# Kernel tuning notes

Hardware: AMD Instinct MI355X
Metric: run time of the kernel (lower is better)

The kernel has to match this reference:

```python
import jax, jax.numpy as jnp
import numpy as np

WIN = 9  # window size per spatial dim (default [9,9,9] for 3D)


def _window_sum(x):
    # Depthwise conv with an all-ones [9,9,9] kernel, stride 1, zero pad 4
    # == sliding-window box sum. lax.reduce_window is the efficient, exact form.
    pad = WIN // 2
    return jax.lax.reduce_window(
        x, 0.0, jax.lax.add,
        window_dimensions=(1, 1, WIN, WIN, WIN),
        window_strides=(1, 1, 1, 1, 1),
        padding=((0, 0), (0, 0), (pad, pad), (pad, pad), (pad, pad)),
    )


def setup_inputs() -> dict:
    key = jax.random.key(0)
    k1, k2 = jax.random.split(key)
    shape = (2, 1, 160, 160, 160)  # [B, C, D, H, W]
    y_true = jax.random.normal(k1, shape, dtype=jnp.float32)
    y_pred = jax.random.normal(k2, shape, dtype=jnp.float32)
    return {"y_true": y_true, "y_pred": y_pred}


def reference(y_true, y_pred):
    Ii, Ji = y_true, y_pred
    win_size = jnp.asarray(WIN ** 3, dtype=Ii.dtype)  # 729

    I2 = Ii * Ii
    J2 = Ji * Ji
    IJ = Ii * Ji

    I_sum = _window_sum(Ii)
    J_sum = _window_sum(Ji)
    I2_sum = _window_sum(I2)
    J2_sum = _window_sum(J2)
    IJ_sum = _window_sum(IJ)

    u_I = I_sum / win_size
    u_J = J_sum / win_size

    cross = IJ_sum - u_J * I_sum - u_I * J_sum + u_I * u_J * win_size
    I_var = I2_sum - 2.0 * u_I * I_sum + u_I * u_I * win_size
    J_var = J2_sum - 2.0 * u_J * J_sum + u_J * u_J * win_size

    cc = cross * cross / (I_var * J_var + 1e-05)
    # mean over spatial dims [2,3,4] -> [B,C], then mean -> scalar
    return (1.0 - jnp.mean(cc, axis=(2, 3, 4))).mean()
```

## Files before the change

kernel.cpp:

```cpp
#include <hip/hip_runtime.h>


typedef float floatx2 __attribute__((ext_vector_type(2)));

constexpr int W = 160, H = 160, D = 160;
constexpr int SLICE = W * H;
constexpr int NVOX  = W * H * D;
constexpr int BATCH = 2;
constexpr int FROW  = 5 * W;
constexpr float RW  = 1.0f / 729.0f;

constexpr int TPB_P = 400;
constexpr int XT    = 80;
constexpr int NXT   = W / XT;
constexpr int CZ    = 80;
constexpr int NCZ   = D / CZ;
constexpr int ZS    = CZ + 8;
constexpr int NUNITS = ZS * 10;
constexpr int NBLK_P = BATCH * H * NXT * NCZ;

constexpr int TPB_Y = 448;
constexpr int YQ    = 40;
constexpr int NYQ   = H / YQ;
constexpr int YR    = YQ + 8;
constexpr int NBLK_Y = BATCH * D * NYQ;
constexpr int LDW   = YR * FROW / 16;

__device__ inline unsigned int pk4(float a, float b, float c, float d) {
    unsigned int u = 0;
    u = __builtin_amdgcn_cvt_pk_fp8_f32(a, b, u, false);
    u = __builtin_amdgcn_cvt_pk_fp8_f32(c, d, u, true);
    return u;
}
__device__ inline void up4(unsigned int v, float* o) {
    floatx2 t;
    t = __builtin_amdgcn_cvt_pk_f32_fp8(v, false); o[0] = t[0]; o[1] = t[1];
    t = __builtin_amdgcn_cvt_pk_f32_fp8(v, true);  o[2] = t[0]; o[3] = t[1];
}
__device__ inline void up8(uint2 v, float* o) {
    up4(v.x, o); up4(v.y, o + 4);
}

__global__ __launch_bounds__(TPB_P) void pass_pzx(const float* __restrict__ I,
                                                  const float* __restrict__ J,
                                                  unsigned char* __restrict__ outA) {
    __shared__ unsigned char xw[5][ZS][XT];

    int blk = blockIdx.x;
    int zc = blk % NCZ;
    int xt = (blk / NCZ) % NXT;
    int y  = (blk / (NCZ * NXT)) % H;
    int b  = blk / (NCZ * NXT * H);
    int tx0 = xt * XT;
    int zbase = zc * CZ - 4;
    const float* Ib = I + (size_t)b * NVOX + y * W;
    const float* Jb = J + (size_t)b * NVOX + y * W;

    const float4 Z4 = make_float4(0.f, 0.f, 0.f, 0.f);
    for (int u = threadIdx.x; u < NUNITS; u += TPB_P) {
        int zs = u / 10;
        int xu = u % 10;
        int gxs = tx0 + xu * 8;
        int gz = zbase + zs;
        float a[16], c[16];
        if (gz >= 0 && gz < D) {
            const float* ip = Ib + (size_t)gz * SLICE + gxs;
            const float* jp = Jb + (size_t)gz * SLICE + gxs;
            float4 A0 = (gxs >= 4)     ? *(const float4*)(ip - 4) : Z4;
            float4 A1 = *(const float4*)(ip);
            float4 A2 = *(const float4*)(ip + 4);
            float4 A3 = (gxs + 11 < W) ? *(const float4*)(ip + 8) : Z4;
            float4 C0 = (gxs >= 4)     ? *(const float4*)(jp - 4) : Z4;
            float4 C1 = *(const float4*)(jp);
            float4 C2 = *(const float4*)(jp + 4);
            float4 C3 = (gxs + 11 < W) ? *(const float4*)(jp + 8) : Z4;
            float at[16] = {A0.x,A0.y,A0.z,A0.w, A1.x,A1.y,A1.z,A1.w,
                            A2.x,A2.y,A2.z,A2.w, A3.x,A3.y,A3.z,A3.w};
            float ct[16] = {C0.x,C0.y,C0.z,C0.w, C1.x,C1.y,C1.z,C1.w,
                            C2.x,C2.y,C2.z,C2.w, C3.x,C3.y,C3.z,C3.w};
#pragma unroll
            for (int k = 0; k < 16; ++k) { a[k] = at[k]; c[k] = ct[k]; }
        } else {
#pragma unroll
            for (int k = 0; k < 16; ++k) { a[k] = 0.f; c[k] = 0.f; }
        }
#pragma unroll
        for (int f = 0; f < 5; ++f) {
            float v[16];
#pragma unroll
            for (int k = 0; k < 16; ++k) {
                float x = a[k], yv = c[k];
                v[k] = (f == 0) ? x : (f == 1) ? yv :
                       (f == 2) ? x * x : (f == 3) ? yv * yv : x * yv;
            }
            float P[16];
            P[0] = v[0];
#pragma unroll
            for (int k = 1; k < 16; ++k) P[k] = P[k - 1] + v[k];
            float w[8];
            w[0] = P[8];
#pragma unroll
            for (int j = 1; j < 8; ++j) w[j] = P[j + 8] - P[j - 1];
            uint2 pk;
            pk.x = pk4(w[0], w[1], w[2], w[3]);
            pk.y = pk4(w[4], w[5], w[6], w[7]);
            *(uint2*)&xw[f][zs][xu * 8] = pk;
        }
    }

    __syncthreads();

    {
        int xg = threadIdx.x % 20;
        int zl = threadIdx.x / 20;
        int x0l = xg * 4;
        int zo0 = zl * 4;

        float acc[5][4];
#pragma unroll
        for (int f = 0; f < 5; ++f)
#pragma unroll
            for (int i = 0; i < 4; ++i) acc[f][i] = 0.f;

#pragma unroll
        for (int k = 0; k < 9; ++k) {
#pragma unroll
            for (int f = 0; f < 5; ++f) {
                unsigned int v = *(const unsigned int*)&xw[f][zo0 + k][x0l];
                float u[4]; up4(v, u);
                acc[f][0] += u[0]; acc[f][1] += u[1];
                acc[f][2] += u[2]; acc[f][3] += u[3];
            }
        }

        int gz0 = zc * CZ + zo0;
        unsigned char* op = outA + ((size_t)(b * D + gz0) * H + y) * FROW + tx0 + x0l;
#pragma unroll
        for (int q = 0; q < 4; ++q) {
#pragma unroll
            for (int f = 0; f < 5; ++f)
                *(unsigned int*)(op + f * W) =
                    pk4(acc[f][0], acc[f][1], acc[f][2], acc[f][3]);
            if (q < 3) {
#pragma unroll
                for (int f = 0; f < 5; ++f) {
                    unsigned int ve = *(const unsigned int*)&xw[f][zo0 + 9 + q][x0l];
                    unsigned int vl = *(const unsigned int*)&xw[f][zo0 + q][x0l];
                    float ue[4], ul[4];
                    up4(ve, ue); up4(vl, ul);
                    acc[f][0] += ue[0] - ul[0]; acc[f][1] += ue[1] - ul[1];
                    acc[f][2] += ue[2] - ul[2]; acc[f][3] += ue[3] - ul[3];
                }
                op += (size_t)H * FROW;
            }
        }
    }
}

__global__ __launch_bounds__(TPB_Y) void pass_y2(const unsigned char* __restrict__ A,
                                                 double* __restrict__ partials) {
    __shared__ unsigned char rows[YR * FROW];
    __shared__ double sm[TPB_Y / 64];

    int blk = blockIdx.x;
    int yq = blk % NYQ;
    int z  = (blk / NYQ) % D;
    int b  = blk / (NYQ * D);
    int y0 = yq * YQ;
    int tid = threadIdx.x;
    const unsigned char* __restrict__ src =
        A + ((size_t)(b * D + z) * H) * FROW;

    for (int i = tid; i < LDW; i += TPB_Y) {
        int off = i * 16;
        int r = off / FROW;
        int gy = y0 - 4 + r;
        uint4 v = make_uint4(0u, 0u, 0u, 0u);
        if (gy >= 0 && gy < H)
            v = *(const uint4*)(src + (size_t)gy * FROW + (off % FROW));
        *(uint4*)&rows[off] = v;
    }
    __syncthreads();

    double acc = 0.0;
    if (tid < 400) {
        int xg = tid % 20;
        int ys = tid / 20;
        int rbase = ys * 2;
        int x8 = xg * 8;

        float s[5][8];
#pragma unroll
        for (int f = 0; f < 5; ++f)
#pragma unroll
            for (int i = 0; i < 8; ++i) s[f][i] = 0.f;

#pragma unroll
        for (int t = 0; t < 9; ++t) {
            const unsigned char* rp = &rows[(rbase + t) * FROW + x8];
#pragma unroll
            for (int f = 0; f < 5; ++f) {
                uint2 v = *(const uint2*)(rp + f * W);
                float u[8]; up8(v, u);
#pragma unroll
                for (int i = 0; i < 8; ++i) s[f][i] += u[i];
            }
        }

#pragma unroll
        for (int o = 0; o < 2; ++o) {
            float rowcc = 0.f;
#pragma unroll
            for (int i = 0; i < 8; ++i) {
                float Is = s[0][i], Js = s[1][i];
                float I2s = s[2][i], J2s = s[3][i], IJs = s[4][i];
                float tI = RW * Is;
                float cross = __builtin_fmaf(-tI, Js, IJs);
                float Iv    = __builtin_fmaf(-tI, Is, I2s);
                float Jv    = __builtin_fmaf(-(RW * Js), Js, J2s);
                float den   = __builtin_fmaf(Iv, Jv, 1e-5f);
                rowcc = __builtin_fmaf(cross * cross, __builtin_amdgcn_rcpf(den), rowcc);
            }
            acc += (double)rowcc;
            if (o == 0) {
                const unsigned char* re = &rows[(rbase + 9) * FROW + x8];
                const unsigned char* rl = &rows[rbase * FROW + x8];
#pragma unroll
                for (int f = 0; f < 5; ++f) {
                    uint2 ve = *(const uint2*)(re + f * W);
                    uint2 vl = *(const uint2*)(rl + f * W);
                    float ue[8], ul[8];
                    up8(ve, ue); up8(vl, ul);
#pragma unroll
                    for (int i = 0; i < 8; ++i) s[f][i] += ue[i] - ul[i];
                }
            }
        }
    }

#pragma unroll
    for (int off = 32; off > 0; off >>= 1) acc += __shfl_down(acc, off);
    if ((tid & 63) == 0) sm[tid >> 6] = acc;
    __syncthreads();
    if (tid == 0) {
        double tt = 0.0;
#pragma unroll
        for (int i = 0; i < TPB_Y / 64; ++i) tt += sm[i];
        partials[blockIdx.x] = tt;
    }
}

__global__ __launch_bounds__(256) void finalize(const double* __restrict__ p,
                                                float* __restrict__ out) {
    double v = 0.0;
    for (int i = threadIdx.x; i < NBLK_Y; i += 256) v += p[i];
#pragma unroll
    for (int off = 32; off > 0; off >>= 1) v += __shfl_down(v, off);
    __shared__ double sm[4];
    int lane = threadIdx.x & 63, wid = threadIdx.x >> 6;
    if (lane == 0) sm[wid] = v;
    __syncthreads();
    if (threadIdx.x == 0) {
        double tt = 0.0;
#pragma unroll
        for (int i = 0; i < 4; ++i) tt += sm[i];
        out[0] = (float)(1.0 - tt / (double)((double)BATCH * (double)NVOX));
    }
}

extern "C" void kernel_launch(void* const* d_in, const int* in_sizes, int n_in,
                              void* d_out, int out_size, void* d_ws, size_t ws_size,
                              hipStream_t stream) {
    const float* I = (const float*)d_in[0];
    const float* J = (const float*)d_in[1];
    float* out = (float*)d_out;

    size_t bufsz = ((size_t)BATCH * 5 * NVOX + 255) / 256 * 256;
    unsigned char* bufA = (unsigned char*)d_ws;
    double* partials = (double*)(bufA + bufsz);

    pass_pzx<<<NBLK_P, TPB_P, 0, stream>>>(I, J, bufA);
    pass_y2<<<NBLK_Y, TPB_Y, 0, stream>>>(bufA, partials);
    finalize<<<1, 256, 0, stream>>>(partials, out);
}
```

Before: 59.64 us.

## Reorder separable box-sum passes: fuse x,y in first pass, do z in second

The first pass now computes the x and y window sums within a single z-slice, reading contiguous rows of a slice instead of strided columns across z. The second pass then does the z window sum and the loss reduction, loading 48 z-planes of one y-row from the fp8 intermediate. This turns the large strided float reads in the first pass into contiguous slice reads. In exchange, the second pass now gathers its rows with a large stride across z from the intermediate buffer.

```diff
diff --git a/kernel.cpp b/kernel.cpp
--- a/kernel.cpp
+++ b/kernel.cpp
@@ -11,20 +11,17 @@
 constexpr float RW  = 1.0f / 729.0f;
 
 constexpr int TPB_P = 400;
-constexpr int XT    = 80;
-constexpr int NXT   = W / XT;
-constexpr int CZ    = 80;
-constexpr int NCZ   = D / CZ;
-constexpr int ZS    = CZ + 8;
-constexpr int NUNITS = ZS * 10;
-constexpr int NBLK_P = BATCH * H * NXT * NCZ;
-
-constexpr int TPB_Y = 448;
-constexpr int YQ    = 40;
-constexpr int NYQ   = H / YQ;
-constexpr int YR    = YQ + 8;
-constexpr int NBLK_Y = BATCH * D * NYQ;
-constexpr int LDW   = YR * FROW / 16;
+constexpr int CHY   = 40, NCHY = H / CHY;
+constexpr int YS    = CHY + 8;
+constexpr int NUNITS = YS * 20;
+constexpr int NBLK_P = BATCH * D * NCHY;
+
+constexpr int TPB_Z2 = 448;
+constexpr int ZQ    = 40;
+constexpr int NZQ   = D / ZQ;
+constexpr int ZR    = ZQ + 8;
+constexpr int NBLK_Z2 = BATCH * H * NZQ;
+constexpr int LDW   = ZR * FROW / 16;
 
 __device__ inline unsigned int pk4(float a, float b, float c, float d) {
     unsigned int u = 0;
@@ -41,31 +38,29 @@
     up4(v.x, o); up4(v.y, o + 4);
 }
 
-__global__ __launch_bounds__(TPB_P) void pass_pzx(const float* __restrict__ I,
+__global__ __launch_bounds__(TPB_P) void pass_pxy(const float* __restrict__ I,
                                                   const float* __restrict__ J,
                                                   unsigned char* __restrict__ outA) {
-    __shared__ unsigned char xw[5][ZS][XT];
+    __shared__ unsigned char xw[5][YS][W];
 
     int blk = blockIdx.x;
-    int zc = blk % NCZ;
-    int xt = (blk / NCZ) % NXT;
-    int y  = (blk / (NCZ * NXT)) % H;
-    int b  = blk / (NCZ * NXT * H);
-    int tx0 = xt * XT;
-    int zbase = zc * CZ - 4;
-    const float* Ib = I + (size_t)b * NVOX + y * W;
-    const float* Jb = J + (size_t)b * NVOX + y * W;
+    int yc = blk % NCHY;
+    int z  = (blk / NCHY) % D;
+    int b  = blk / (NCHY * D);
+    int y0 = yc * CHY;
+    const float* Ib = I + (size_t)b * NVOX + (size_t)z * SLICE;
+    const float* Jb = J + (size_t)b * NVOX + (size_t)z * SLICE;
 
     const float4 Z4 = make_float4(0.f, 0.f, 0.f, 0.f);
     for (int u = threadIdx.x; u < NUNITS; u += TPB_P) {
-        int zs = u / 10;
-        int xu = u % 10;
-        int gxs = tx0 + xu * 8;
-        int gz = zbase + zs;
+        int r  = u / 20;
+        int xu = u % 20;
+        int gxs = xu * 8;
+        int gy = y0 - 4 + r;
         float a[16], c[16];
-        if (gz >= 0 && gz < D) {
-            const float* ip = Ib + (size_t)gz * SLICE + gxs;
-            const float* jp = Jb + (size_t)gz * SLICE + gxs;
+        if (gy >= 0 && gy < H) {
+            const float* ip = Ib + (size_t)gy * W + gxs;
+            const float* jp = Jb + (size_t)gy * W + gxs;
             float4 A0 = (gxs >= 4)     ? *(const float4*)(ip - 4) : Z4;
             float4 A1 = *(const float4*)(ip);
             float4 A2 = *(const float4*)(ip + 4);
@@ -104,17 +99,17 @@
             uint2 pk;
             pk.x = pk4(w[0], w[1], w[2], w[3]);
             pk.y = pk4(w[4], w[5], w[6], w[7]);
-            *(uint2*)&xw[f][zs][xu * 8] = pk;
+            *(uint2*)&xw[f][r][xu * 8] = pk;
         }
     }
 
     __syncthreads();
 
     {
-        int xg = threadIdx.x % 20;
-        int zl = threadIdx.x / 20;
+        int xg = threadIdx.x % 40;
+        int yl = threadIdx.x / 40;
         int x0l = xg * 4;
-        int zo0 = zl * 4;
+        int yo0 = yl * 4;
 
         float acc[5][4];
 #pragma unroll
@@ -126,15 +121,14 @@
         for (int k = 0; k < 9; ++k) {
 #pragma unroll
             for (int f = 0; f < 5; ++f) {
-                unsigned int v = *(const unsigned int*)&xw[f][zo0 + k][x0l];
+                unsigned int v = *(const unsigned int*)&xw[f][yo0 + k][x0l];
                 float u[4]; up4(v, u);
                 acc[f][0] += u[0]; acc[f][1] += u[1];
                 acc[f][2] += u[2]; acc[f][3] += u[3];
             }
         }
 
-        int gz0 = zc * CZ + zo0;
-        unsigned char* op = outA + ((size_t)(b * D + gz0) * H + y) * FROW + tx0 + x0l;
+        unsigned char* op = outA + ((size_t)(b * D + z) * H + (y0 + yo0)) * FROW + x0l;
 #pragma unroll
         for (int q = 0; q < 4; ++q) {
 #pragma unroll
@@ -144,40 +138,38 @@
             if (q < 3) {
 #pragma unroll
                 for (int f = 0; f < 5; ++f) {
-                    unsigned int ve = *(const unsigned int*)&xw[f][zo0 + 9 + q][x0l];
-                    unsigned int vl = *(const unsigned int*)&xw[f][zo0 + q][x0l];
+                    unsigned int ve = *(const unsigned int*)&xw[f][yo0 + 9 + q][x0l];
+                    unsigned int vl = *(const unsigned int*)&xw[f][yo0 + q][x0l];
                     float ue[4], ul[4];
                     up4(ve, ue); up4(vl, ul);
                     acc[f][0] += ue[0] - ul[0]; acc[f][1] += ue[1] - ul[1];
                     acc[f][2] += ue[2] - ul[2]; acc[f][3] += ue[3] - ul[3];
                 }
-                op += (size_t)H * FROW;
-            }
-        }
-    }
-}
-
-__global__ __launch_bounds__(TPB_Y) void pass_y2(const unsigned char* __restrict__ A,
-                                                 double* __restrict__ partials) {
-    __shared__ unsigned char rows[YR * FROW];
-    __shared__ double sm[TPB_Y / 64];
+                op += FROW;
+            }
+        }
+    }
+}
+
+__global__ __launch_bounds__(TPB_Z2) void pass_z2(const unsigned char* __restrict__ A,
+                                                  double* __restrict__ partials) {
+    __shared__ unsigned char rows[ZR * FROW];
+    __shared__ double sm[TPB_Z2 / 64];
 
     int blk = blockIdx.x;
-    int yq = blk % NYQ;
-    int z  = (blk / NYQ) % D;
-    int b  = blk / (NYQ * D);
-    int y0 = yq * YQ;
+    int zq = blk % NZQ;
+    int y  = (blk / NZQ) % H;
+    int b  = blk / (NZQ * H);
+    int z0 = zq * ZQ;
     int tid = threadIdx.x;
-    const unsigned char* __restrict__ src =
-        A + ((size_t)(b * D + z) * H) * FROW;
-
-    for (int i = tid; i < LDW; i += TPB_Y) {
+
+    for (int i = tid; i < LDW; i += TPB_Z2) {
         int off = i * 16;
         int r = off / FROW;
-        int gy = y0 - 4 + r;
+        int gz = z0 - 4 + r;
         uint4 v = make_uint4(0u, 0u, 0u, 0u);
-        if (gy >= 0 && gy < H)
-            v = *(const uint4*)(src + (size_t)gy * FROW + (off % FROW));
+        if (gz >= 0 && gz < D)
+            v = *(const uint4*)(A + ((size_t)(b * D + gz) * H + y) * FROW + (off % FROW));
         *(uint4*)&rows[off] = v;
     }
     __syncthreads();
@@ -185,8 +177,8 @@
     double acc = 0.0;
     if (tid < 400) {
         int xg = tid % 20;
-        int ys = tid / 20;
-        int rbase = ys * 2;
+        int zs = tid / 20;
+        int rbase = zs * 2;
         int x8 = xg * 8;
 
         float s[5][8];
@@ -245,7 +237,7 @@
     if (tid == 0) {
         double tt = 0.0;
 #pragma unroll
-        for (int i = 0; i < TPB_Y / 64; ++i) tt += sm[i];
+        for (int i = 0; i < TPB_Z2 / 64; ++i) tt += sm[i];
         partials[blockIdx.x] = tt;
     }
 }
@@ -253,7 +245,7 @@
 __global__ __launch_bounds__(256) void finalize(const double* __restrict__ p,
                                                 float* __restrict__ out) {
     double v = 0.0;
-    for (int i = threadIdx.x; i < NBLK_Y; i += 256) v += p[i];
+    for (int i = threadIdx.x; i < NBLK_Z2; i += 256) v += p[i];
 #pragma unroll
     for (int off = 32; off > 0; off >>= 1) v += __shfl_down(v, off);
     __shared__ double sm[4];
@@ -279,7 +271,7 @@
     unsigned char* bufA = (unsigned char*)d_ws;
     double* partials = (double*)(bufA + bufsz);
 
-    pass_pzx<<<NBLK_P, TPB_P, 0, stream>>>(I, J, bufA);
-    pass_y2<<<NBLK_Y, TPB_Y, 0, stream>>>(bufA, partials);
+    pass_pxy<<<NBLK_P, TPB_P, 0, stream>>>(I, J, bufA);
+    pass_z2<<<NBLK_Z2, TPB_Z2, 0, stream>>>(bufA, partials);
     finalize<<<1, 256, 0, stream>>>(partials, out);
 }
```

Measured after the change: 70.96 us. 19.0% more time.

## Shrink z-chunk in pzx pass and stage x-window sums in bf16 LDS

Applied to the files above, without the earlier changes.

The first pass now covers 32 z-slices per block instead of 80, using 320 threads, and each thread produces 2 z outputs instead of 4. This creates many more blocks for better occupancy and load balance. In exchange, the 8-slice halo is a larger share of each chunk, so there are more redundant global reads and less sliding-window reuse. The x-window partial sums kept in shared memory change from fp8 to bf16, which improves intermediate precision and simplifies unpacking. The cost is double the LDS footprint per element and wider shared-memory loads.

```diff
diff --git a/kernel.cpp b/kernel.cpp
--- a/kernel.cpp
+++ b/kernel.cpp
@@ -10,13 +10,12 @@
 constexpr int FROW  = 5 * W;
 constexpr float RW  = 1.0f / 729.0f;
 
-constexpr int TPB_P = 400;
+constexpr int TPB_P = 320;
 constexpr int XT    = 80;
 constexpr int NXT   = W / XT;
-constexpr int CZ    = 80;
+constexpr int CZ    = 32;
 constexpr int NCZ   = D / CZ;
 constexpr int ZS    = CZ + 8;
-constexpr int NUNITS = ZS * 10;
 constexpr int NBLK_P = BATCH * H * NXT * NCZ;
 
 constexpr int TPB_Y = 448;
@@ -40,11 +39,25 @@
 __device__ inline void up8(uint2 v, float* o) {
     up4(v.x, o); up4(v.y, o + 4);
 }
+__device__ inline unsigned short f2bf(float f) {
+    unsigned int u = __builtin_bit_cast(unsigned int, f);
+    u += 0x7fffu + ((u >> 16) & 1u);
+    return (unsigned short)(u >> 16);
+}
+__device__ inline unsigned int bfpack2(float lo, float hi) {
+    return (unsigned int)f2bf(lo) | ((unsigned int)f2bf(hi) << 16);
+}
+__device__ inline float bflo(unsigned int u) {
+    return __builtin_bit_cast(float, u << 16);
+}
+__device__ inline float bfhi(unsigned int u) {
+    return __builtin_bit_cast(float, u & 0xffff0000u);
+}
 
 __global__ __launch_bounds__(TPB_P) void pass_pzx(const float* __restrict__ I,
                                                   const float* __restrict__ J,
                                                   unsigned char* __restrict__ outA) {
-    __shared__ unsigned char xw[5][ZS][XT];
+    __shared__ unsigned short xw[5][ZS][XT];
 
     int blk = blockIdx.x;
     int zc = blk % NCZ;
@@ -57,7 +70,7 @@
     const float* Jb = J + (size_t)b * NVOX + y * W;
 
     const float4 Z4 = make_float4(0.f, 0.f, 0.f, 0.f);
-    for (int u = threadIdx.x; u < NUNITS; u += TPB_P) {
+    for (int u = threadIdx.x; u < ZS * 10; u += TPB_P) {
         int zs = u / 10;
         int xu = u % 10;
         int gxs = tx0 + xu * 8;
@@ -66,14 +79,14 @@
         if (gz >= 0 && gz < D) {
             const float* ip = Ib + (size_t)gz * SLICE + gxs;
             const float* jp = Jb + (size_t)gz * SLICE + gxs;
-            float4 A0 = (gxs >= 4)     ? *(const float4*)(ip - 4) : Z4;
+            float4 A0 = (gxs >= 4)      ? *(const float4*)(ip - 4) : Z4;
             float4 A1 = *(const float4*)(ip);
             float4 A2 = *(const float4*)(ip + 4);
-            float4 A3 = (gxs + 11 < W) ? *(const float4*)(ip + 8) : Z4;
-            float4 C0 = (gxs >= 4)     ? *(const float4*)(jp - 4) : Z4;
+            float4 A3 = (gxs + 11 < W)  ? *(const float4*)(ip + 8) : Z4;
+            float4 C0 = (gxs >= 4)      ? *(const float4*)(jp - 4) : Z4;
             float4 C1 = *(const float4*)(jp);
             float4 C2 = *(const float4*)(jp + 4);
-            float4 C3 = (gxs + 11 < W) ? *(const float4*)(jp + 8) : Z4;
+            float4 C3 = (gxs + 11 < W)  ? *(const float4*)(jp + 8) : Z4;
             float at[16] = {A0.x,A0.y,A0.z,A0.w, A1.x,A1.y,A1.z,A1.w,
                             A2.x,A2.y,A2.z,A2.w, A3.x,A3.y,A3.z,A3.w};
             float ct[16] = {C0.x,C0.y,C0.z,C0.w, C1.x,C1.y,C1.z,C1.w,
@@ -102,59 +115,58 @@
 #pragma unroll
             for (int j = 1; j < 8; ++j) w[j] = P[j + 8] - P[j - 1];
             uint2 pk;
-            pk.x = pk4(w[0], w[1], w[2], w[3]);
-            pk.y = pk4(w[4], w[5], w[6], w[7]);
-            *(uint2*)&xw[f][zs][xu * 8] = pk;
-        }
-    }
-
-    __syncthreads();
-
-    {
-        int xg = threadIdx.x % 20;
-        int zl = threadIdx.x / 20;
-        int x0l = xg * 4;
-        int zo0 = zl * 4;
-
-        float acc[5][4];
-#pragma unroll
-        for (int f = 0; f < 5; ++f)
-#pragma unroll
-            for (int i = 0; i < 4; ++i) acc[f][i] = 0.f;
-
-#pragma unroll
-        for (int k = 0; k < 9; ++k) {
-#pragma unroll
-            for (int f = 0; f < 5; ++f) {
-                unsigned int v = *(const unsigned int*)&xw[f][zo0 + k][x0l];
-                float u[4]; up4(v, u);
-                acc[f][0] += u[0]; acc[f][1] += u[1];
-                acc[f][2] += u[2]; acc[f][3] += u[3];
-            }
-        }
-
-        int gz0 = zc * CZ + zo0;
-        unsigned char* op = outA + ((size_t)(b * D + gz0) * H + y) * FROW + tx0 + x0l;
-#pragma unroll
-        for (int q = 0; q < 4; ++q) {
-#pragma unroll
-            for (int f = 0; f < 5; ++f)
-                *(unsigned int*)(op + f * W) =
-                    pk4(acc[f][0], acc[f][1], acc[f][2], acc[f][3]);
-            if (q < 3) {
-#pragma unroll
-                for (int f = 0; f < 5; ++f) {
-                    unsigned int ve = *(const unsigned int*)&xw[f][zo0 + 9 + q][x0l];
-                    unsigned int vl = *(const unsigned int*)&xw[f][zo0 + q][x0l];
-                    float ue[4], ul[4];
-                    up4(ve, ue); up4(vl, ul);
-                    acc[f][0] += ue[0] - ul[0]; acc[f][1] += ue[1] - ul[1];
-                    acc[f][2] += ue[2] - ul[2]; acc[f][3] += ue[3] - ul[3];
-                }
-                op += (size_t)H * FROW;
-            }
-        }
-    }
+            pk.x = bfpack2(w[0], w[1]);
+            pk.y = bfpack2(w[2], w[3]);
+            uint2 pk2;
+            pk2.x = bfpack2(w[4], w[5]);
+            pk2.y = bfpack2(w[6], w[7]);
+            *(uint2*)&xw[f][zs][xu * 8]     = pk;
+            *(uint2*)&xw[f][zs][xu * 8 + 4] = pk2;
+        }
+    }
+
+    __syncthreads();
+
+    int xg = threadIdx.x % 20;
+    int zl = threadIdx.x / 20;
+    int x0l = xg * 4;
+    int zo0 = zl * 2;
+
+    float acc[5][4];
+#pragma unroll
+    for (int f = 0; f < 5; ++f)
+#pragma unroll
+        for (int i = 0; i < 4; ++i) acc[f][i] = 0.f;
+
+#pragma unroll
+    for (int k = 0; k < 9; ++k) {
+#pragma unroll
+        for (int f = 0; f < 5; ++f) {
+            uint2 v = *(const uint2*)&xw[f][zo0 + k][x0l];
+            acc[f][0] += bflo(v.x); acc[f][1] += bfhi(v.x);
+            acc[f][2] += bflo(v.y); acc[f][3] += bfhi(v.y);
+        }
+    }
+
+    int gz0 = zc * CZ + zo0;
+    unsigned char* op0 = outA + ((size_t)(b * D + gz0) * H + y) * FROW + tx0 + x0l;
+#pragma unroll
+    for (int f = 0; f < 5; ++f)
+        *(unsigned int*)(op0 + f * W) = pk4(acc[f][0], acc[f][1], acc[f][2], acc[f][3]);
+
+#pragma unroll
+    for (int f = 0; f < 5; ++f) {
+        uint2 ve = *(const uint2*)&xw[f][zo0 + 9][x0l];
+        uint2 vl = *(const uint2*)&xw[f][zo0][x0l];
+        acc[f][0] += bflo(ve.x) - bflo(vl.x);
+        acc[f][1] += bfhi(ve.x) - bfhi(vl.x);
+        acc[f][2] += bflo(ve.y) - bflo(vl.y);
+        acc[f][3] += bfhi(ve.y) - bfhi(vl.y);
+    }
+    unsigned char* op1 = op0 + (size_t)H * FROW;
+#pragma unroll
+    for (int f = 0; f < 5; ++f)
+        *(unsigned int*)(op1 + f * W) = pk4(acc[f][0], acc[f][1], acc[f][2], acc[f][3]);
 }
 
 __global__ __launch_bounds__(TPB_Y) void pass_y2(const unsigned char* __restrict__ A,
```

After: 64.42 us. 1.08x slower.

## Split fused x/z box-sum pass into separate x and z passes via intermediate buffer

Applied to the files above, without the earlier changes.

Replaces the fused pass that did the x-window sum and the z-window sum in shared memory with two kernels. The first computes x-window sums per row and writes fp8 results in a transposed (b,y,z) layout. The second loads contiguous z-rows into shared memory and writes z-summed data in the layout the y pass expects. The aim is to remove strided z-gathers from the original fp32 inputs and to get coalesced, fully parallel per-row work, at the cost of an extra fp8 intermediate buffer round trip and one more kernel launch.

```diff
diff --git a/kernel.cpp b/kernel.cpp
--- a/kernel.cpp
+++ b/kernel.cpp
@@ -10,21 +10,24 @@
 constexpr int FROW  = 5 * W;
 constexpr float RW  = 1.0f / 729.0f;
 
-constexpr int TPB_P = 400;
-constexpr int XT    = 80;
-constexpr int NXT   = W / XT;
-constexpr int CZ    = 80;
-constexpr int NCZ   = D / CZ;
-constexpr int ZS    = CZ + 8;
-constexpr int NUNITS = ZS * 10;
-constexpr int NBLK_P = BATCH * H * NXT * NCZ;
+constexpr int TPB_X = 256;
+constexpr int XU    = W / 8;
+constexpr int NTH_X = BATCH * D * H * XU;
+constexpr int NBLK_X = NTH_X / TPB_X;
+
+constexpr int TPB_Z = 448;
+constexpr int ZQ    = 40;
+constexpr int NZQ   = D / ZQ;
+constexpr int ZR    = ZQ + 8;
+constexpr int NBLK_Z = BATCH * H * NZQ;
+constexpr int LDWZ  = ZR * FROW / 16;
 
 constexpr int TPB_Y = 448;
 constexpr int YQ    = 40;
 constexpr int NYQ   = H / YQ;
 constexpr int YR    = YQ + 8;
 constexpr int NBLK_Y = BATCH * D * NYQ;
-constexpr int LDW   = YR * FROW / 16;
+constexpr int LDWY  = YR * FROW / 16;
 
 __device__ inline unsigned int pk4(float a, float b, float c, float d) {
     unsigned int u = 0;
@@ -41,117 +44,133 @@
     up4(v.x, o); up4(v.y, o + 4);
 }
 
-__global__ __launch_bounds__(TPB_P) void pass_pzx(const float* __restrict__ I,
-                                                  const float* __restrict__ J,
-                                                  unsigned char* __restrict__ outA) {
-    __shared__ unsigned char xw[5][ZS][XT];
+__global__ __launch_bounds__(TPB_X) void pass_x(const float* __restrict__ I,
+                                                const float* __restrict__ J,
+                                                unsigned char* __restrict__ outA) {
+    int t = blockIdx.x * TPB_X + threadIdx.x;
+    int xu  = t % XU;
+    int row = t / XU;
+    int y = row % H;
+    int zb = row / H;
+    int z = zb % D;
+    int b = zb / D;
+    int x0 = xu * 8;
+
+    const float* ip = I + (size_t)row * W + x0;
+    const float* jp = J + (size_t)row * W + x0;
+    const float4 Z4 = make_float4(0.f, 0.f, 0.f, 0.f);
+    bool hasL = xu > 0, hasR = xu < XU - 1;
+
+    float4 a0 = hasL ? *(const float4*)(ip - 4) : Z4;
+    float4 a1 = *(const float4*)(ip);
+    float4 a2 = *(const float4*)(ip + 4);
+    float4 a3 = hasR ? *(const float4*)(ip + 8) : Z4;
+    float4 c0 = hasL ? *(const float4*)(jp - 4) : Z4;
+    float4 c1 = *(const float4*)(jp);
+    float4 c2 = *(const float4*)(jp + 4);
+    float4 c3 = hasR ? *(const float4*)(jp + 8) : Z4;
+
+    float a[16] = {a0.x,a0.y,a0.z,a0.w, a1.x,a1.y,a1.z,a1.w,
+                   a2.x,a2.y,a2.z,a2.w, a3.x,a3.y,a3.z,a3.w};
+    float c[16] = {c0.x,c0.y,c0.z,c0.w, c1.x,c1.y,c1.z,c1.w,
+                   c2.x,c2.y,c2.z,c2.w, c3.x,c3.y,c3.z,c3.w};
+
+    unsigned char* op = outA + ((size_t)(b * H + y) * D + z) * FROW + x0;
+#pragma unroll
+    for (int f = 0; f < 5; ++f) {
+        float v[16];
+#pragma unroll
+        for (int k = 0; k < 16; ++k) {
+            float x = a[k], yv = c[k];
+            v[k] = (f == 0) ? x : (f == 1) ? yv :
+                   (f == 2) ? x * x : (f == 3) ? yv * yv : x * yv;
+        }
+        float P[16];
+        P[0] = v[0];
+#pragma unroll
+        for (int k = 1; k < 16; ++k) P[k] = P[k - 1] + v[k];
+        float w[8];
+        w[0] = P[8];
+#pragma unroll
+        for (int j = 1; j < 8; ++j) w[j] = P[j + 8] - P[j - 1];
+        uint2 pk;
+        pk.x = pk4(w[0], w[1], w[2], w[3]);
+        pk.y = pk4(w[4], w[5], w[6], w[7]);
+        *(uint2*)(op + f * W) = pk;
+    }
+}
+
+__global__ __launch_bounds__(TPB_Z) void pass_z2(const unsigned char* __restrict__ A,
+                                                 unsigned char* __restrict__ B) {
+    __shared__ unsigned char rows[ZR * FROW];
 
     int blk = blockIdx.x;
-    int zc = blk % NCZ;
-    int xt = (blk / NCZ) % NXT;
-    int y  = (blk / (NCZ * NXT)) % H;
-    int b  = blk / (NCZ * NXT * H);
-    int tx0 = xt * XT;
-    int zbase = zc * CZ - 4;
-    const float* Ib = I + (size_t)b * NVOX + y * W;
-    const float* Jb = J + (size_t)b * NVOX + y * W;
-
-    const float4 Z4 = make_float4(0.f, 0.f, 0.f, 0.f);
-    for (int u = threadIdx.x; u < NUNITS; u += TPB_P) {
-        int zs = u / 10;
-        int xu = u % 10;
-        int gxs = tx0 + xu * 8;
-        int gz = zbase + zs;
-        float a[16], c[16];
-        if (gz >= 0 && gz < D) {
-            const float* ip = Ib + (size_t)gz * SLICE + gxs;
-            const float* jp = Jb + (size_t)gz * SLICE + gxs;
-            float4 A0 = (gxs >= 4)     ? *(const float4*)(ip - 4) : Z4;
-            float4 A1 = *(const float4*)(ip);
-            float4 A2 = *(const float4*)(ip + 4);
-            float4 A3 = (gxs + 11 < W) ? *(const float4*)(ip + 8) : Z4;
-            float4 C0 = (gxs >= 4)     ? *(const float4*)(jp - 4) : Z4;
-            float4 C1 = *(const float4*)(jp);
-            float4 C2 = *(const float4*)(jp + 4);
-            float4 C3 = (gxs + 11 < W) ? *(const float4*)(jp + 8) : Z4;
-            float at[16] = {A0.x,A0.y,A0.z,A0.w, A1.x,A1.y,A1.z,A1.w,
-                            A2.x,A2.y,A2.z,A2.w, A3.x,A3.y,A3.z,A3.w};
-            float ct[16] = {C0.x,C0.y,C0.z,C0.w, C1.x,C1.y,C1.z,C1.w,
-                            C2.x,C2.y,C2.z,C2.w, C3.x,C3.y,C3.z,C3.w};
-#pragma unroll
-            for (int k = 0; k < 16; ++k) { a[k] = at[k]; c[k] = ct[k]; }
-        } else {
-#pragma unroll
-            for (int k = 0; k < 16; ++k) { a[k] = 0.f; c[k] = 0.f; }
-        }
-#pragma unroll
-        for (int f = 0; f < 5; ++f) {
-            float v[16];
-#pragma unroll
-            for (int k = 0; k < 16; ++k) {
-                float x = a[k], yv = c[k];
-                v[k] = (f == 0) ? x : (f == 1) ? yv :
-                       (f == 2) ? x * x : (f == 3) ? yv * yv : x * yv;
-            }
-            float P[16];
-            P[0] = v[0];
-#pragma unroll
-            for (int k = 1; k < 16; ++k) P[k] = P[k - 1] + v[k];
-            float w[8];
-            w[0] = P[8];
-#pragma unroll
-            for (int j = 1; j < 8; ++j) w[j] = P[j + 8] - P[j - 1];
-            uint2 pk;
-            pk.x = pk4(w[0], w[1], w[2], w[3]);
-            pk.y = pk4(w[4], w[5], w[6], w[7]);
-            *(uint2*)&xw[f][zs][xu * 8] = pk;
-        }
-    }
-
+    int zq = blk % NZQ;
+    int y  = (blk / NZQ) % H;
+    int b  = blk / (NZQ * H);
+    int z0 = zq * ZQ;
+    int tid = threadIdx.x;
+    const unsigned char* __restrict__ src =
+        A + ((size_t)(b * H + y) * D) * FROW;
+
+    for (int i = tid; i < LDWZ; i += TPB_Z) {
+        int off = i * 16;
+        int r = off / FROW;
+        int gz = z0 - 4 + r;
+        uint4 v = make_uint4(0u, 0u, 0u, 0u);
+        if (gz >= 0 && gz < D)
+            v = *(const uint4*)(src + (size_t)gz * FROW + (off % FROW));
+        *(uint4*)&rows[off] = v;
+    }
     __syncthreads();
 
-    {
-        int xg = threadIdx.x % 20;
-        int zl = threadIdx.x / 20;
-        int x0l = xg * 4;
-        int zo0 = zl * 4;
-
-        float acc[5][4];
+    if (tid < 400) {
+        int xg = tid % 20;
+        int zs = tid / 20;
+        int rbase = zs * 2;
+        int x8 = xg * 8;
+
+        float s[5][8];
 #pragma unroll
         for (int f = 0; f < 5; ++f)
 #pragma unroll
-            for (int i = 0; i < 4; ++i) acc[f][i] = 0.f;
-
-#pragma unroll
-        for (int k = 0; k < 9; ++k) {
+            for (int i = 0; i < 8; ++i) s[f][i] = 0.f;
+
+#pragma unroll
+        for (int tt = 0; tt < 9; ++tt) {
+            const unsigned char* rp = &rows[(rbase + tt) * FROW + x8];
 #pragma unroll
             for (int f = 0; f < 5; ++f) {
-                unsigned int v = *(const unsigned int*)&xw[f][zo0 + k][x0l];
-                float u[4]; up4(v, u);
-                acc[f][0] += u[0]; acc[f][1] += u[1];
-                acc[f][2] += u[2]; acc[f][3] += u[3];
-            }
-        }
-
-        int gz0 = zc * CZ + zo0;
-        unsigned char* op = outA + ((size_t)(b * D + gz0) * H + y) * FROW + tx0 + x0l;
-#pragma unroll
-        for (int q = 0; q < 4; ++q) {
-#pragma unroll
-            for (int f = 0; f < 5; ++f)
-                *(unsigned int*)(op + f * W) =
-                    pk4(acc[f][0], acc[f][1], acc[f][2], acc[f][3]);
-            if (q < 3) {
+                uint2 v = *(const uint2*)(rp + f * W);
+                float u[8]; up8(v, u);
+#pragma unroll
+                for (int i = 0; i < 8; ++i) s[f][i] += u[i];
+            }
+        }
+
+#pragma unroll
+        for (int o = 0; o < 2; ++o) {
+            int gzo = z0 + rbase + o;
+            unsigned char* op = B + ((size_t)(b * D + gzo) * H + y) * FROW + x8;
+#pragma unroll
+            for (int f = 0; f < 5; ++f) {
+                uint2 pk;
+                pk.x = pk4(s[f][0], s[f][1], s[f][2], s[f][3]);
+                pk.y = pk4(s[f][4], s[f][5], s[f][6], s[f][7]);
+                *(uint2*)(op + f * W) = pk;
+            }
+            if (o == 0) {
+                const unsigned char* re = &rows[(rbase + 9) * FROW + x8];
+                const unsigned char* rl = &rows[rbase * FROW + x8];
 #pragma unroll
                 for (int f = 0; f < 5; ++f) {
-                    unsigned int ve = *(const unsigned int*)&xw[f][zo0 + 9 + q][x0l];
-                    unsigned int vl = *(const unsigned int*)&xw[f][zo0 + q][x0l];
-                    float ue[4], ul[4];
-                    up4(ve, ue); up4(vl, ul);
-                    acc[f][0] += ue[0] - ul[0]; acc[f][1] += ue[1] - ul[1];
-                    acc[f][2] += ue[2] - ul[2]; acc[f][3] += ue[3] - ul[3];
+                    uint2 ve = *(const uint2*)(re + f * W);
+                    uint2 vl = *(const uint2*)(rl + f * W);
+                    float ue[8], ul[8];
+                    up8(ve, ue); up8(vl, ul);
+#pragma unroll
+                    for (int i = 0; i < 8; ++i) s[f][i] += ue[i] - ul[i];
                 }
-                op += (size_t)H * FROW;
             }
         }
     }
@@ -171,7 +190,7 @@
     const unsigned char* __restrict__ src =
         A + ((size_t)(b * D + z) * H) * FROW;
 
-    for (int i = tid; i < LDW; i += TPB_Y) {
+    for (int i = tid; i < LDWY; i += TPB_Y) {
         int off = i * 16;
         int r = off / FROW;
         int gy = y0 - 4 + r;
@@ -277,9 +296,11 @@
 
     size_t bufsz = ((size_t)BATCH * 5 * NVOX + 255) / 256 * 256;
     unsigned char* bufA = (unsigned char*)d_ws;
-    double* partials = (double*)(bufA + bufsz);
-
-    pass_pzx<<<NBLK_P, TPB_P, 0, stream>>>(I, J, bufA);
-    pass_y2<<<NBLK_Y, TPB_Y, 0, stream>>>(bufA, partials);
+    unsigned char* bufB = bufA + bufsz;
+    double* partials = (double*)(bufB + bufsz);
+
+    pass_x<<<NBLK_X, TPB_X, 0, stream>>>(I, J, bufA);
+    pass_z2<<<NBLK_Z, TPB_Z, 0, stream>>>(bufA, bufB);
+    pass_y2<<<NBLK_Y, TPB_Y, 0, stream>>>(bufB, partials);
     finalize<<<1, 256, 0, stream>>>(partials, out);
 }
```

New measurement: 82.89 us. +39.0%, slower.
